# Optimization experiments

Measured on AMD Instinct MI355X. Metric: run time of the kernel, lower is better.

Reference implementation:

```python
import math
import jax, jax.numpy as jnp
import numpy as np

N = 20000      # nodes
E = 320000     # edges
D_IN = 256
D_OUT = 256
H = 8
DK = D_OUT // H  # 32


def setup_inputs() -> dict:
    key = jax.random.key(0)
    ks = jax.random.split(key, 16)
    h = jax.random.normal(ks[0], (N, D_IN), dtype=jnp.float32)
    src = jax.random.randint(ks[1], (E,), 0, N, dtype=jnp.int32)
    dst = jax.random.randint(ks[2], (E,), 0, N, dtype=jnp.int32)
    s = 1.0 / math.sqrt(D_IN)
    Wk = jax.random.uniform(ks[3], (D_OUT, D_IN), jnp.float32, -s, s)
    bk = jnp.zeros((D_OUT,), jnp.float32)
    Wq = jax.random.uniform(ks[4], (D_OUT, D_IN), jnp.float32, -s, s)
    bq = jnp.zeros((D_OUT,), jnp.float32)
    Wv = jax.random.uniform(ks[5], (D_OUT, D_IN), jnp.float32, -s, s)
    bv = jnp.zeros((D_OUT,), jnp.float32)
    so = 1.0 / math.sqrt(D_OUT)
    Wa = jax.random.uniform(ks[6], (D_OUT, D_OUT), jnp.float32, -so, so)
    ba = jnp.zeros((D_OUT,), jnp.float32)
    # xavier_uniform over [n_rel=1, H, DK, DK]; fan_in = fan_out = DK
    bound = math.sqrt(6.0 / (DK + DK))
    rel_att = jax.random.uniform(ks[7], (H, DK, DK), jnp.float32, -bound, bound)
    rel_msg = jax.random.uniform(ks[8], (H, DK, DK), jnp.float32, -bound, bound)
    rel_pri = jnp.ones((H,), jnp.float32)
    skip = jnp.ones((), jnp.float32)
    return {"h": h, "src": src, "dst": dst, "Wk": Wk, "bk": bk, "Wq": Wq,
            "bq": bq, "Wv": Wv, "bv": bv, "Wa": Wa, "ba": ba,
            "rel_att": rel_att, "rel_msg": rel_msg, "rel_pri": rel_pri,
            "skip": skip}


def reference(h, src, dst, Wk, bk, Wq, bq, Wv, bv, Wa, ba, rel_att, rel_msg, rel_pri, skip):
    n = h.shape[0]
    sqrt_dk = math.sqrt(DK)
    # per-node projections, [N, H, DK]
    k = (h @ Wk.T + bk).reshape(n, H, DK)
    q = (h @ Wq.T + bq).reshape(n, H, DK)
    v = (h @ Wv.T + bv).reshape(n, H, DK)
    # relation-specific transforms (single relation, index 0)
    k = jnp.einsum('nhd,hde->nhe', k, rel_att)
    v = jnp.einsum('nhd,hde->nhe', v, rel_msg)
    # edge-wise dot-product score: v_dot_u(q_dst, k_src) -> [E, H]
    score = jnp.einsum('ehd,ehd->eh', q[dst], k[src]) * rel_pri / sqrt_dk
    # edge softmax normalized by dst
    m = jax.ops.segment_max(score, dst, num_segments=n)          # [N, H]
    ex = jnp.exp(score - m[dst])
    z = jax.ops.segment_sum(ex, dst, num_segments=n)             # [N, H]
    attn = ex / z[dst]                                           # [E, H]
    # weighted message aggregation: sum_e attn * v_src -> [N, H, DK]
    agg = jax.ops.segment_sum(v[src] * attn[:, :, None], dst, num_segments=n)
    t = agg.reshape(n, D_OUT)
    trans = t @ Wa.T + ba                                        # dropout = eval identity
    alpha = jax.nn.sigmoid(skip)
    return trans * alpha + h * (1.0 - alpha)
```

## Files before the change

### kernel.cpp

```cpp
#include <hip/hip_runtime.h>
#include <hip/hip_bf16.h>
#include <math.h>


#define NN   20000
#define NE   320000
#define MPAD 20096

typedef unsigned short u16;
typedef unsigned char  u8;
typedef __bf16 bf16x8 __attribute__((ext_vector_type(8)));
typedef u16    u16x8  __attribute__((ext_vector_type(8)));
typedef float  f32x4  __attribute__((ext_vector_type(4)));

__device__ __forceinline__ float bf2f(u16 x) {
    union { float f; unsigned u; } c; c.u = ((unsigned)x) << 16; return c.f;
}
__device__ __forceinline__ u16 f2bf(float f) {
    union { float f; unsigned u; } c; c.f = f;
    unsigned r = c.u + 0x7fffu + ((c.u >> 16) & 1u);
    return (u16)(r >> 16);
}

#if __has_builtin(__builtin_amdgcn_cvt_pk_fp8_f32) && __has_builtin(__builtin_amdgcn_cvt_pk_f32_fp8)
#define HWFP8 1
#else
#define HWFP8 0
#endif

__device__ __forceinline__ u8 f2fp8(float x) {
#if HWFP8
    return (u8)(__builtin_amdgcn_cvt_pk_fp8_f32(x, x, 0, false) & 0xff);
#else
    if (x != x) return 0x7f;
    unsigned sg = (x < 0.f) ? 0x80u : 0u;
    float a = fabsf(x); if (a > 448.f) a = 448.f;
    if (a < 0.015625f) {
        int m = (int)rintf(a * 512.f);
        if (m > 7) return (u8)(sg | 0x08);
        return (u8)(sg | m);
    }
    int e; (void)frexpf(a, &e);
    int p = e - 1;
    float mant = a * exp2f((float)(-p));
    int m = (int)rintf((mant - 1.f) * 8.f);
    int ef = p + 7;
    if (m == 8) { m = 0; ef++; }
    if (ef > 15) { ef = 15; m = 6; }
    return (u8)(sg | (ef << 3) | m);
#endif
}

__device__ __forceinline__ void fp8x4_dec(unsigned w, float* o) {
#if HWFP8
    auto lo = __builtin_amdgcn_cvt_pk_f32_fp8(w, false);
    auto hi = __builtin_amdgcn_cvt_pk_f32_fp8(w, true);
    o[0] = lo[0]; o[1] = lo[1]; o[2] = hi[0]; o[3] = hi[1];
#else
    #pragma unroll
    for (int j = 0; j < 4; ++j) {
        u8 b = (w >> (8 * j)) & 0xff;
        unsigned e = (b >> 3) & 15, m = b & 7;
        float v;
        if (e) { union { unsigned u; float f; } c; c.u = ((e + 120) << 23) | (m << 20); v = c.f; }
        else v = (float)m * 0.001953125f;
        o[j] = (b & 0x80) ? -v : v;
    }
#endif
}

__device__ __forceinline__ float fast_exp2(float x) {
#if __has_builtin(__builtin_amdgcn_exp2f)
    return __builtin_amdgcn_exp2f(x);
#else
    return exp2f(x);
#endif
}

__device__ __forceinline__ void gload_lds16(const void* g, void* l) {
    __builtin_amdgcn_global_load_lds(
        (const __attribute__((address_space(1))) unsigned*)g,
        (__attribute__((address_space(3))) unsigned*)l, 16, 0, 0);
}

__global__ void prep0(const float* __restrict__ Wq, const float* __restrict__ bq,
                      const float* __restrict__ Wk, const float* __restrict__ bk,
                      const float* __restrict__ Wv, const float* __restrict__ bv,
                      const float* __restrict__ Wa,
                      const float* __restrict__ rel_att, const float* __restrict__ rel_msg,
                      const float* __restrict__ rel_pri,
                      u16* __restrict__ W_all, float* __restrict__ b_eff,
                      u16* __restrict__ Wa_bf, int* __restrict__ deg)
{
    const int bid = blockIdx.x, t = threadIdx.x;
    if (bid < 20) {
        const int i = bid * 256 + t;
        if (i < 5024) *(int4*)(deg + i * 4) = make_int4(0, 0, 0, 0);
    } else if (bid < 788) {
        const int row = bid - 20, col = t;
        float val;
        if (row < 256) {
            val = Wq[row * 256 + col];
            if (col == 0) b_eff[row] = bq[row];
        } else {
            const int i = row - 256, g = i >> 7, o = i & 127;
            const bool isk = (o < 64);
            const int d = 64 * g + (isk ? o : o - 64);
            const int hh = d >> 5, e = d & 31;
            if (isk) {
                const float s = rel_pri[hh] * 0.17677669529663687f * 1.4426950408889634f;
                float acc = 0.f;
                for (int dd = 0; dd < 32; ++dd)
                    acc += rel_att[hh * 1024 + dd * 32 + e] * Wk[(hh * 32 + dd) * 256 + col];
                val = acc * s;
                if (col == 0) {
                    float b = 0.f;
                    for (int dd = 0; dd < 32; ++dd) b += rel_att[hh * 1024 + dd * 32 + e] * bk[hh * 32 + dd];
                    b_eff[row] = b * s;
                }
            } else {
                float acc = 0.f;
                for (int dd = 0; dd < 32; ++dd)
                    acc += rel_msg[hh * 1024 + dd * 32 + e] * Wv[(hh * 32 + dd) * 256 + col];
                val = acc;
                if (col == 0) {
                    float b = 0.f;
                    for (int dd = 0; dd < 32; ++dd) b += rel_msg[hh * 1024 + dd * 32 + e] * bv[hh * 32 + dd];
                    b_eff[row] = b;
                }
            }
        }
        W_all[row * 256 + col] = f2bf(val);
    } else {
        const int idx = (bid - 788) * 256 + t;
        Wa_bf[idx] = f2bf(Wa[idx]);
    }
}

__global__ __launch_bounds__(256) void gemm_qkv(
    const float* __restrict__ h, const u16* __restrict__ B,
    const float* __restrict__ bias, const int* __restrict__ dst,
    u16* __restrict__ qb, u8* __restrict__ kv8, int* __restrict__ deg)
{
    if (blockIdx.x >= 960) {
        const int e = (blockIdx.x - 960) * 256 + threadIdx.x;
        if (e < NE) atomicAdd(&deg[dst[e]], 1);
        return;
    }
    const int xcd = blockIdx.x & 7, slot = blockIdx.x >> 3;
    const int rb = (slot % 20) * 8 + xcd;
    const int cb = slot / 20;
    if (rb >= 157) return;
    __shared__ u16 LDS[128 * 128];
    u16* At = LDS;
    u16* Bt = LDS + 128 * 64;
    const int t = threadIdx.x;
    const int wave = t >> 6, lane = t & 63;
    const int row0 = rb * 128, col0 = cb * 128;
    const int wm = (wave >> 1) * 64, wn = (wave & 1) * 64;
    const int cl = lane & 15, rh = lane >> 4;
    const int srow = t >> 3;
    const int lchunk = t & 7;
    const int swz = (t >> 3) & 7;
    const int scol = lchunk * 8;
    const int sc_swz = (lchunk ^ swz) * 8;

    f32x4 acc[4][4] = {};

    for (int k0 = 0; k0 < 256; k0 += 64) {
        __syncthreads();
        #pragma unroll
        for (int r = 0; r < 4; ++r) {
            const int rT = r * 32 + srow;
            const int grow = row0 + rT;
            u16x8 w8 = (u16x8)0;
            if (grow < NN) {
                const float4 f0 = *(const float4*)(h + (size_t)grow * 256 + k0 + scol);
                const float4 f1 = *(const float4*)(h + (size_t)grow * 256 + k0 + scol + 4);
                w8[0] = f2bf(f0.x); w8[1] = f2bf(f0.y); w8[2] = f2bf(f0.z); w8[3] = f2bf(f0.w);
                w8[4] = f2bf(f1.x); w8[5] = f2bf(f1.y); w8[6] = f2bf(f1.z); w8[7] = f2bf(f1.w);
            }
            *(u16x8*)&At[rT * 64 + (lchunk ^ swz) * 8] = w8;
            gload_lds16(B + (size_t)(col0 + rT) * 256 + k0 + sc_swz,
                        &Bt[(r * 256 + wave * 64) * 8]);
        }
        __syncthreads();
        #pragma unroll
        for (int kk = 0; kk < 64; kk += 32) {
            const int kc = kk >> 3;
            bf16x8 af[4], bb[4];
            #pragma unroll
            for (int m = 0; m < 4; ++m) {
                const int ar = wm + 16 * m + cl;
                af[m] = *(const bf16x8*)&At[ar * 64 + (((kc + rh) ^ (ar & 7)) * 8)];
            }
            #pragma unroll
            for (int n = 0; n < 4; ++n) {
                const int br = wn + 16 * n + cl;
                bb[n] = *(const bf16x8*)&Bt[br * 64 + (((kc + rh) ^ (br & 7)) * 8)];
            }
            #pragma unroll
            for (int m = 0; m < 4; ++m)
                #pragma unroll
                for (int n = 0; n < 4; ++n)
                    acc[m][n] = __builtin_amdgcn_mfma_f32_16x16x32_bf16(af[m], bb[n], acc[m][n], 0, 0, 0);
        }
    }

    __syncthreads();
    if (cb < 2) {
        #pragma unroll
        for (int n = 0; n < 4; ++n) {
            const int col = wn + 16 * n + cl;
            const float bv = bias[col0 + col];
            #pragma unroll
            for (int m = 0; m < 4; ++m) {
                const int rowb = wm + 16 * m + 4 * rh;
                #pragma unroll
                for (int r = 0; r < 4; ++r) {
                    const int row = rowb + r;
                    LDS[row * 128 + ((((col >> 3) ^ (row & 15)) << 3) | (col & 7))] =
                        f2bf(acc[m][n][r] + bv);
                }
            }
        }
        __syncthreads();
        #pragma unroll
        for (int it = 0; it < 8; ++it) {
            const int u = it * 256 + t;
            const int row = u >> 4, lc = u & 15;
            *(u16x8*)(qb + (size_t)(row0 + row) * 256 + col0 + lc * 8) =
                *(const u16x8*)&LDS[row * 128 + ((lc ^ (row & 15)) << 3)];
        }
    } else {
        u8* Cs8 = (u8*)LDS;
        const int g = cb - 2;
        #pragma unroll
        for (int n = 0; n < 4; ++n) {
            const int col = wn + 16 * n + cl;
            const float bv = bias[col0 + col];
            const int o = col & 63;
            const int p = ((o >> 3) << 4) + ((col < 64) ? 0 : 8) + (o & 7);
            #pragma unroll
            for (int m = 0; m < 4; ++m) {
                const int rowb = wm + 16 * m + 4 * rh;
                #pragma unroll
                for (int r = 0; r < 4; ++r) {
                    const int row = rowb + r;
                    Cs8[row * 128 + ((((p >> 3) ^ (row & 15)) << 3) | (p & 7))] =
                        f2fp8(acc[m][n][r] + bv);
                }
            }
        }
        __syncthreads();
        #pragma unroll
        for (int it = 0; it < 4; ++it) {
            const int u = it * 256 + t;
            const int row = u >> 3, un = u & 7;
            const uint2 a = *(const uint2*)&Cs8[row * 128 + (((2 * un) ^ (row & 15)) << 3)];
            const uint2 b = *(const uint2*)&Cs8[row * 128 + (((2 * un + 1) ^ (row & 15)) << 3)];
            *(uint4*)(kv8 + (size_t)(row0 + row) * 512 + g * 128 + un * 16) =
                make_uint4(a.x, a.y, b.x, b.y);
        }
    }
}

__global__ __launch_bounds__(256) void gemm_out(
    const u16* __restrict__ A, const u16* __restrict__ B,
    const float* __restrict__ bias, const float* __restrict__ hres,
    const float* __restrict__ skip, float* __restrict__ C)
{
    const int xcd = blockIdx.x & 7, slot = blockIdx.x >> 3;
    const int rb = (slot % 40) * 8 + xcd;
    const int cbo = slot / 40;
    if (rb >= 314) return;
    __shared__ u16 At[64 * 64];
    __shared__ u16 Bt[64 * 64];
    const int t = threadIdx.x;
    const int wave = t >> 6, lane = t & 63;
    const int row0 = rb * 64, col0 = cbo * 64;
    const int wm = (wave >> 1) * 32, wn = (wave & 1) * 32;
    const int cl = lane & 15, rh = lane >> 4;
    const int srow = t >> 3;
    const int sc_swz = (((t & 7) ^ ((t >> 3) & 7))) * 8;

    f32x4 acc[2][2] = {};

    for (int k0 = 0; k0 < 256; k0 += 64) {
        __syncthreads();
        #pragma unroll
        for (int r = 0; r < 2; ++r) {
            const int rowT = r * 32 + srow;
            gload_lds16(A + (size_t)(row0 + rowT) * 256 + k0 + sc_swz, &At[(r * 2048 + wave * 512)]);
            gload_lds16(B + (size_t)(col0 + rowT) * 256 + k0 + sc_swz, &Bt[(r * 2048 + wave * 512)]);
        }
        __syncthreads();
        #pragma unroll
        for (int kk = 0; kk < 64; kk += 32) {
            const int kc = kk >> 3;
            bf16x8 af[2], bb[2];
            #pragma unroll
            for (int m = 0; m < 2; ++m) {
                const int ar = wm + 16 * m + cl;
                af[m] = *(const bf16x8*)&At[ar * 64 + (((kc + rh) ^ (ar & 7)) * 8)];
            }
            #pragma unroll
            for (int n = 0; n < 2; ++n) {
                const int br = wn + 16 * n + cl;
                bb[n] = *(const bf16x8*)&Bt[br * 64 + (((kc + rh) ^ (br & 7)) * 8)];
            }
            #pragma unroll
            for (int m = 0; m < 2; ++m)
                #pragma unroll
                for (int n = 0; n < 2; ++n)
                    acc[m][n] = __builtin_amdgcn_mfma_f32_16x16x32_bf16(af[m], bb[n], acc[m][n], 0, 0, 0);
        }
    }
    const float alpha = 1.f / (1.f + __expf(-skip[0]));
    const float beta = 1.f - alpha;
    #pragma unroll
    for (int n = 0; n < 2; ++n) {
        const int col = col0 + wn + 16 * n + cl;
        const float bv = bias[col];
        #pragma unroll
        for (int m = 0; m < 2; ++m) {
            const int rowb = row0 + wm + 16 * m + 4 * rh;
            #pragma unroll
            for (int r = 0; r < 4; ++r) {
                const int row = rowb + r;
                if (row < NN)
                    C[(size_t)row * 256 + col] =
                        (acc[m][n][r] + bv) * alpha + hres[(size_t)row * 256 + col] * beta;
            }
        }
    }
}

__global__ __launch_bounds__(1024) void scan1(const int* __restrict__ deg,
                                              int* __restrict__ off, int* __restrict__ bsum)
{
    __shared__ int wsum[16];
    __shared__ int wpre[16];
    const int t = threadIdx.x, b = blockIdx.x;
    const int i = b * 1024 + t;
    const int lane = t & 63, wv = t >> 6;
    const int v = (i < NN) ? deg[i] : 0;
    int s = v;
    #pragma unroll
    for (int o = 1; o < 64; o <<= 1) {
        const int u = __shfl_up(s, o);
        if (lane >= o) s += u;
    }
    if (lane == 63) wsum[wv] = s;
    __syncthreads();
    if (wv == 0) {
        const int x = (lane < 16) ? wsum[lane] : 0;
        int sx = x;
        #pragma unroll
        for (int o = 1; o < 16; o <<= 1) {
            const int u = __shfl_up(sx, o);
            if (lane >= o) sx += u;
        }
        if (lane < 16) wpre[lane] = sx - x;
    }
    __syncthreads();
    const int incl = s + wpre[wv];
    if (i < NN) off[i] = incl - v;
    if (t == 1023) bsum[b] = incl;
}

__global__ __launch_bounds__(1024) void scan2(const int* __restrict__ bsum,
                                              int* __restrict__ off, int* __restrict__ cur)
{
    __shared__ int pre;
    const int t = threadIdx.x, b = blockIdx.x;
    const int i = b * 1024 + t;
    if (t == 0) {
        int p = 0;
        for (int j = 0; j < b; ++j) p += bsum[j];
        pre = p;
    }
    __syncthreads();
    if (i < NN) {
        const int o = off[i] + pre;
        off[i] = o; cur[i] = o;
    }
    if (b == 19 && t == 0) off[NN] = pre + bsum[19];
}

__global__ void scatter_edges(const int* __restrict__ dst, const int* __restrict__ src,
                              int* __restrict__ cur, int* __restrict__ esrc)
{
    const int e = blockIdx.x * 256 + threadIdx.x;
    if (e < NE) {
        const int p = atomicAdd(&cur[dst[e]], 1);
        esrc[p] = src[e];
    }
}

__device__ __forceinline__ void agg_edge(const u8* __restrict__ kv8, int id,
                                         const float* qf, int sl, float& z, float* acc)
{
    const uint4 w = *(const uint4*)(kv8 + (size_t)id * 512 + sl * 16);
    float kf[8], vf[8];
    fp8x4_dec(w.x, kf); fp8x4_dec(w.y, kf + 4);
    float s = 0.f;
    #pragma unroll
    for (int j = 0; j < 8; ++j) s += qf[j] * kf[j];
    s += __shfl_xor(s, 1);
    s += __shfl_xor(s, 2);
    const float ex = fast_exp2(s);
    z += ex;
    fp8x4_dec(w.z, vf); fp8x4_dec(w.w, vf + 4);
    #pragma unroll
    for (int j = 0; j < 8; ++j) acc[j] += ex * vf[j];
}

__global__ __launch_bounds__(256) void aggregate(
    const u16* __restrict__ qb, const u8* __restrict__ kv8, const int* __restrict__ off,
    const int* __restrict__ esrc, u16* __restrict__ tout)
{
    const int wid = blockIdx.x * 4 + (threadIdx.x >> 6);
    const int lane = threadIdx.x & 63;
    const int half = lane >> 5, sl = lane & 31;
    if (wid >= MPAD) return;
    if (wid >= NN) {
        if (half == 0) *(u16x8*)(tout + (size_t)wid * 256 + sl * 8) = (u16x8)0;
        return;
    }
    const u16x8 qv = *(const u16x8*)(qb + (size_t)wid * 256 + sl * 8);
    float qf[8];
    #pragma unroll
    for (int j = 0; j < 8; ++j) qf[j] = bf2f(qv[j]);
    float acc[8] = {0.f, 0.f, 0.f, 0.f, 0.f, 0.f, 0.f, 0.f};
    float z = 0.f;
    const int e0 = off[wid], e1 = off[wid + 1];
    for (int c0 = e0; c0 < e1; c0 += 64) {
        const int cnt = min(64, e1 - c0);
        const int jj = c0 + lane;
        const int myid = (jj < e1) ? esrc[jj] : 0;
        for (int i = 0; i < cnt; i += 16) {
            int ii[8], idv[8];
            #pragma unroll
            for (int j = 0; j < 8; ++j) {
                ii[j] = i + 2 * j + half;
                idv[j] = __shfl(myid, ii[j]);
            }
            #pragma unroll
            for (int j = 0; j < 8; ++j)
                if (ii[j] < cnt)
                    agg_edge(kv8, idv[j], qf, sl, z, acc);
        }
    }
    #pragma unroll
    for (int j = 0; j < 8; ++j) acc[j] += __shfl_xor(acc[j], 32);
    z += __shfl_xor(z, 32);
    if (half == 0) {
        const float rz = (z > 0.f) ? 1.f / z : 0.f;
        u16x8 o;
        #pragma unroll
        for (int j = 0; j < 8; ++j) o[j] = f2bf(acc[j] * rz);
        *(u16x8*)(tout + (size_t)wid * 256 + sl * 8) = o;
    }
}

extern "C" void kernel_launch(void* const* d_in, const int* in_sizes, int n_in,
                              void* d_out, int out_size, void* d_ws, size_t ws_size,
                              hipStream_t stream)
{
    const float* h   = (const float*)d_in[0];
    const int*   src = (const int*)d_in[1];
    const int*   dst = (const int*)d_in[2];
    const float* Wk  = (const float*)d_in[3];
    const float* bk  = (const float*)d_in[4];
    const float* Wq  = (const float*)d_in[5];
    const float* bq  = (const float*)d_in[6];
    const float* Wv  = (const float*)d_in[7];
    const float* bv  = (const float*)d_in[8];
    const float* Wa  = (const float*)d_in[9];
    const float* ba  = (const float*)d_in[10];
    const float* rel_att = (const float*)d_in[11];
    const float* rel_msg = (const float*)d_in[12];
    const float* rel_pri = (const float*)d_in[13];
    const float* skip    = (const float*)d_in[14];
    float* out = (float*)d_out;

    char* w = (char*)d_ws;
    u16*   W_all = (u16*)(w + 0);
    float* b_eff = (float*)(w + 393216);
    u16*   Wa_bf = (u16*)(w + 396288);
    u16*   qb    = (u16*)(w + 527360);
    u8*    kv8   = (u8*)(w + 10816512);
    u16*   t_bf  = (u16*)(w + 21105664);
    int*   deg   = (int*)(w + 31394816);
    int*   off   = (int*)(w + 31475200);
    int*   cur   = (int*)(w + 31555584);
    int*   bsum  = (int*)(w + 31635968);
    int*   esrc  = (int*)(w + 31636096);

    prep0<<<1044, 256, 0, stream>>>(Wq, bq, Wk, bk, Wv, bv, Wa,
                                    rel_att, rel_msg, rel_pri,
                                    W_all, b_eff, Wa_bf, deg);
    gemm_qkv<<<960 + 1250, 256, 0, stream>>>(h, W_all, b_eff, dst, qb, kv8, deg);
    scan1<<<20, 1024, 0, stream>>>(deg, off, bsum);
    scan2<<<20, 1024, 0, stream>>>(bsum, off, cur);
    scatter_edges<<<NE / 256, 256, 0, stream>>>(dst, src, cur, esrc);
    aggregate<<<MPAD / 4, 256, 0, stream>>>(qb, kv8, off, esrc, t_bf);
    gemm_out<<<1280, 256, 0, stream>>>(t_bf, Wa_bf, ba, h, skip, out);
}
```

Before: 107.6 us.

## Double-buffer LDS tiles in QKV and output GEMMs, move degree count to prep

Both GEMM kernels now prefetch the next K-slice into a second LDS buffer while MFMAs run on the current one, which removes one barrier per iteration and overlaps global loads with compute. The degree histogram atomics move from the QKV GEMM launch into the prep kernel, and the degree buffer is cleared with a memset instead of prep blocks. The QKV GEMM doubles its LDS footprint to 64KB, which may reduce occupancy, and the memset adds an extra queued operation.

```diff
diff --git a/kernel.cpp b/kernel.cpp
--- a/kernel.cpp
+++ b/kernel.cpp
@@ -88,16 +88,13 @@
                       const float* __restrict__ Wv, const float* __restrict__ bv,
                       const float* __restrict__ Wa,
                       const float* __restrict__ rel_att, const float* __restrict__ rel_msg,
-                      const float* __restrict__ rel_pri,
+                      const float* __restrict__ rel_pri, const int* __restrict__ dst,
                       u16* __restrict__ W_all, float* __restrict__ b_eff,
                       u16* __restrict__ Wa_bf, int* __restrict__ deg)
 {
     const int bid = blockIdx.x, t = threadIdx.x;
-    if (bid < 20) {
-        const int i = bid * 256 + t;
-        if (i < 5024) *(int4*)(deg + i * 4) = make_int4(0, 0, 0, 0);
-    } else if (bid < 788) {
-        const int row = bid - 20, col = t;
+    if (bid < 768) {
+        const int row = bid, col = t;
         float val;
         if (row < 256) {
             val = Wq[row * 256 + col];
@@ -131,29 +128,24 @@
             }
         }
         W_all[row * 256 + col] = f2bf(val);
+    } else if (bid < 1024) {
+        const int idx = (bid - 768) * 256 + t;
+        Wa_bf[idx] = f2bf(Wa[idx]);
     } else {
-        const int idx = (bid - 788) * 256 + t;
-        Wa_bf[idx] = f2bf(Wa[idx]);
+        const int e = (bid - 1024) * 256 + t;
+        if (e < NE) atomicAdd(&deg[dst[e]], 1);
     }
 }
 
 __global__ __launch_bounds__(256) void gemm_qkv(
     const float* __restrict__ h, const u16* __restrict__ B,
-    const float* __restrict__ bias, const int* __restrict__ dst,
-    u16* __restrict__ qb, u8* __restrict__ kv8, int* __restrict__ deg)
-{
-    if (blockIdx.x >= 960) {
-        const int e = (blockIdx.x - 960) * 256 + threadIdx.x;
-        if (e < NE) atomicAdd(&deg[dst[e]], 1);
-        return;
-    }
+    const float* __restrict__ bias, u16* __restrict__ qb, u8* __restrict__ kv8)
+{
     const int xcd = blockIdx.x & 7, slot = blockIdx.x >> 3;
     const int rb = (slot % 20) * 8 + xcd;
     const int cb = slot / 20;
     if (rb >= 157) return;
-    __shared__ u16 LDS[128 * 128];
-    u16* At = LDS;
-    u16* Bt = LDS + 128 * 64;
+    __shared__ u16 LDS[32768];
     const int t = threadIdx.x;
     const int wave = t >> 6, lane = t & 63;
     const int row0 = rb * 128, col0 = cb * 128;
@@ -166,28 +158,55 @@
     const int sc_swz = (lchunk ^ swz) * 8;
 
     f32x4 acc[4][4] = {};
-
-    for (int k0 = 0; k0 < 256; k0 += 64) {
-        __syncthreads();
-        #pragma unroll
-        for (int r = 0; r < 4; ++r) {
-            const int rT = r * 32 + srow;
-            const int grow = row0 + rT;
-            u16x8 w8 = (u16x8)0;
-            if (grow < NN) {
-                const float4 f0 = *(const float4*)(h + (size_t)grow * 256 + k0 + scol);
-                const float4 f1 = *(const float4*)(h + (size_t)grow * 256 + k0 + scol + 4);
-                w8[0] = f2bf(f0.x); w8[1] = f2bf(f0.y); w8[2] = f2bf(f0.z); w8[3] = f2bf(f0.w);
-                w8[4] = f2bf(f1.x); w8[5] = f2bf(f1.y); w8[6] = f2bf(f1.z); w8[7] = f2bf(f1.w);
-            }
-            *(u16x8*)&At[rT * 64 + (lchunk ^ swz) * 8] = w8;
-            gload_lds16(B + (size_t)(col0 + rT) * 256 + k0 + sc_swz,
-                        &Bt[(r * 256 + wave * 64) * 8]);
-        }
-        __syncthreads();
-        #pragma unroll
-        for (int kk = 0; kk < 64; kk += 32) {
-            const int kc = kk >> 3;
+    float4 fa[4][2];
+
+    #pragma unroll
+    for (int r = 0; r < 4; ++r) {
+        const int grow = row0 + r * 32 + srow;
+        if (grow < NN) {
+            fa[r][0] = *(const float4*)(h + (size_t)grow * 256 + scol);
+            fa[r][1] = *(const float4*)(h + (size_t)grow * 256 + scol + 4);
+        } else {
+            fa[r][0] = make_float4(0.f, 0.f, 0.f, 0.f);
+            fa[r][1] = make_float4(0.f, 0.f, 0.f, 0.f);
+        }
+        gload_lds16(B + (size_t)(col0 + r * 32 + srow) * 256 + sc_swz,
+                    &LDS[8192 + (r * 256 + wave * 64) * 8]);
+    }
+    #pragma unroll
+    for (int r = 0; r < 4; ++r) {
+        u16x8 w8;
+        w8[0] = f2bf(fa[r][0].x); w8[1] = f2bf(fa[r][0].y); w8[2] = f2bf(fa[r][0].z); w8[3] = f2bf(fa[r][0].w);
+        w8[4] = f2bf(fa[r][1].x); w8[5] = f2bf(fa[r][1].y); w8[6] = f2bf(fa[r][1].z); w8[7] = f2bf(fa[r][1].w);
+        *(u16x8*)&LDS[(r * 32 + srow) * 64 + (lchunk ^ swz) * 8] = w8;
+    }
+    __syncthreads();
+
+    #pragma unroll
+    for (int ki = 0; ki < 4; ++ki) {
+        const int boff = (ki & 1) * 16384;
+        const int nboff = boff ^ 16384;
+        if (ki < 3) {
+            const int k0n = (ki + 1) * 64;
+            #pragma unroll
+            for (int r = 0; r < 4; ++r) {
+                const int grow = row0 + r * 32 + srow;
+                if (grow < NN) {
+                    fa[r][0] = *(const float4*)(h + (size_t)grow * 256 + k0n + scol);
+                    fa[r][1] = *(const float4*)(h + (size_t)grow * 256 + k0n + scol + 4);
+                } else {
+                    fa[r][0] = make_float4(0.f, 0.f, 0.f, 0.f);
+                    fa[r][1] = make_float4(0.f, 0.f, 0.f, 0.f);
+                }
+                gload_lds16(B + (size_t)(col0 + r * 32 + srow) * 256 + k0n + sc_swz,
+                            &LDS[nboff + 8192 + (r * 256 + wave * 64) * 8]);
+            }
+        }
+        const u16* At = &LDS[boff];
+        const u16* Bt = &LDS[boff + 8192];
+        #pragma unroll
+        for (int kk = 0; kk < 2; ++kk) {
+            const int kc = kk * 4;
             bf16x8 af[4], bb[4];
             #pragma unroll
             for (int m = 0; m < 4; ++m) {
@@ -205,9 +224,18 @@
                 for (int n = 0; n < 4; ++n)
                     acc[m][n] = __builtin_amdgcn_mfma_f32_16x16x32_bf16(af[m], bb[n], acc[m][n], 0, 0, 0);
         }
-    }
-
-    __syncthreads();
+        if (ki < 3) {
+            #pragma unroll
+            for (int r = 0; r < 4; ++r) {
+                u16x8 w8;
+                w8[0] = f2bf(fa[r][0].x); w8[1] = f2bf(fa[r][0].y); w8[2] = f2bf(fa[r][0].z); w8[3] = f2bf(fa[r][0].w);
+                w8[4] = f2bf(fa[r][1].x); w8[5] = f2bf(fa[r][1].y); w8[6] = f2bf(fa[r][1].z); w8[7] = f2bf(fa[r][1].w);
+                *(u16x8*)&LDS[nboff + (r * 32 + srow) * 64 + (lchunk ^ swz) * 8] = w8;
+            }
+        }
+        __syncthreads();
+    }
+
     if (cb < 2) {
         #pragma unroll
         for (int n = 0; n < 4; ++n) {
@@ -272,32 +300,46 @@
 {
     const int xcd = blockIdx.x & 7, slot = blockIdx.x >> 3;
     const int rb = (slot % 40) * 8 + xcd;
-    const int cbo = slot / 40;
+    const int cb = slot / 40;
     if (rb >= 314) return;
-    __shared__ u16 At[64 * 64];
-    __shared__ u16 Bt[64 * 64];
+    __shared__ u16 LDS[16384];
     const int t = threadIdx.x;
     const int wave = t >> 6, lane = t & 63;
-    const int row0 = rb * 64, col0 = cbo * 64;
+    const int row0 = rb * 64, col0 = cb * 64;
     const int wm = (wave >> 1) * 32, wn = (wave & 1) * 32;
     const int cl = lane & 15, rh = lane >> 4;
     const int srow = t >> 3;
     const int sc_swz = (((t & 7) ^ ((t >> 3) & 7))) * 8;
 
+    #pragma unroll
+    for (int r = 0; r < 2; ++r) {
+        const int rowT = r * 32 + srow;
+        gload_lds16(A + (size_t)(row0 + rowT) * 256 + sc_swz, &LDS[(r * 2048 + wave * 512)]);
+        gload_lds16(B + (size_t)(col0 + rowT) * 256 + sc_swz, &LDS[4096 + (r * 2048 + wave * 512)]);
+    }
+    __syncthreads();
+
     f32x4 acc[2][2] = {};
-
-    for (int k0 = 0; k0 < 256; k0 += 64) {
-        __syncthreads();
-        #pragma unroll
-        for (int r = 0; r < 2; ++r) {
-            const int rowT = r * 32 + srow;
-            gload_lds16(A + (size_t)(row0 + rowT) * 256 + k0 + sc_swz, &At[(r * 2048 + wave * 512)]);
-            gload_lds16(B + (size_t)(col0 + rowT) * 256 + k0 + sc_swz, &Bt[(r * 2048 + wave * 512)]);
-        }
-        __syncthreads();
-        #pragma unroll
-        for (int kk = 0; kk < 64; kk += 32) {
-            const int kc = kk >> 3;
+    #pragma unroll
+    for (int ki = 0; ki < 4; ++ki) {
+        const int boff = (ki & 1) * 8192;
+        const int nboff = boff ^ 8192;
+        if (ki < 3) {
+            const int k0n = (ki + 1) * 64;
+            #pragma unroll
+            for (int r = 0; r < 2; ++r) {
+                const int rowT = r * 32 + srow;
+                gload_lds16(A + (size_t)(row0 + rowT) * 256 + k0n + sc_swz,
+                            &LDS[nboff + (r * 2048 + wave * 512)]);
+                gload_lds16(B + (size_t)(col0 + rowT) * 256 + k0n + sc_swz,
+                            &LDS[nboff + 4096 + (r * 2048 + wave * 512)]);
+            }
+        }
+        const u16* At = &LDS[boff];
+        const u16* Bt = &LDS[boff + 4096];
+        #pragma unroll
+        for (int kk = 0; kk < 2; ++kk) {
+            const int kc = kk * 4;
             bf16x8 af[2], bb[2];
             #pragma unroll
             for (int m = 0; m < 2; ++m) {
@@ -315,6 +357,7 @@
                 for (int n = 0; n < 2; ++n)
                     acc[m][n] = __builtin_amdgcn_mfma_f32_16x16x32_bf16(af[m], bb[n], acc[m][n], 0, 0, 0);
         }
+        __syncthreads();
     }
     const float alpha = 1.f / (1.f + __expf(-skip[0]));
     const float beta = 1.f - alpha;
@@ -498,10 +541,11 @@
     int*   bsum  = (int*)(w + 31635968);
     int*   esrc  = (int*)(w + 31636096);
 
-    prep0<<<1044, 256, 0, stream>>>(Wq, bq, Wk, bk, Wv, bv, Wa,
-                                    rel_att, rel_msg, rel_pri,
-                                    W_all, b_eff, Wa_bf, deg);
-    gemm_qkv<<<960 + 1250, 256, 0, stream>>>(h, W_all, b_eff, dst, qb, kv8, deg);
+    (void)hipMemsetAsync(deg, 0, NN * sizeof(int), stream);
+    prep0<<<1024 + 1250, 256, 0, stream>>>(Wq, bq, Wk, bk, Wv, bv, Wa,
+                                           rel_att, rel_msg, rel_pri, dst,
+                                           W_all, b_eff, Wa_bf, deg);
+    gemm_qkv<<<960, 256, 0, stream>>>(h, W_all, b_eff, qb, kv8);
     scan1<<<20, 1024, 0, stream>>>(deg, off, bsum);
     scan2<<<20, 1024, 0, stream>>>(bsum, off, cur);
     scatter_edges<<<NE / 256, 256, 0, stream>>>(dst, src, cur, esrc);
```

Result: slower. 115.1 us (+7.0%).

## Register-prefetch next K tile in both GEMMs to overlap loads with MFMA

Applied to the files above, without the earlier changes.

Both the fused projection GEMM and the output GEMM drop the direct global-to-LDS loads. Each K step now prefetches the next 64-wide tile into registers, runs the MFMAs on the current LDS tile, then writes the prefetched data into LDS with the same XOR swizzle. The aim is to hide global load latency behind compute instead of stalling at a barrier on every K step. In exchange it raises register pressure, since fp32 A values and bf16 B vectors stay live across the MFMA loop, and it adds a barrier around each LDS commit.

```diff
diff --git a/kernel.cpp b/kernel.cpp
--- a/kernel.cpp
+++ b/kernel.cpp
@@ -75,12 +75,6 @@
 #else
     return exp2f(x);
 #endif
-}
-
-__device__ __forceinline__ void gload_lds16(const void* g, void* l) {
-    __builtin_amdgcn_global_load_lds(
-        (const __attribute__((address_space(1))) unsigned*)g,
-        (__attribute__((address_space(3))) unsigned*)l, 16, 0, 0);
 }
 
 __global__ void prep0(const float* __restrict__ Wq, const float* __restrict__ bq,
@@ -161,33 +155,46 @@
     const int cl = lane & 15, rh = lane >> 4;
     const int srow = t >> 3;
     const int lchunk = t & 7;
-    const int swz = (t >> 3) & 7;
-    const int scol = lchunk * 8;
-    const int sc_swz = (lchunk ^ swz) * 8;
+    const int swz = srow & 7;
 
     f32x4 acc[4][4] = {};
-
-    for (int k0 = 0; k0 < 256; k0 += 64) {
-        __syncthreads();
+    float4 a0[4], a1[4];
+    u16x8 bz[4];
+
+    auto LOAD = [&](int k0) {
         #pragma unroll
         for (int r = 0; r < 4; ++r) {
-            const int rT = r * 32 + srow;
-            const int grow = row0 + rT;
-            u16x8 w8 = (u16x8)0;
+            const int grow = row0 + r * 32 + srow;
             if (grow < NN) {
-                const float4 f0 = *(const float4*)(h + (size_t)grow * 256 + k0 + scol);
-                const float4 f1 = *(const float4*)(h + (size_t)grow * 256 + k0 + scol + 4);
-                w8[0] = f2bf(f0.x); w8[1] = f2bf(f0.y); w8[2] = f2bf(f0.z); w8[3] = f2bf(f0.w);
-                w8[4] = f2bf(f1.x); w8[5] = f2bf(f1.y); w8[6] = f2bf(f1.z); w8[7] = f2bf(f1.w);
-            }
-            *(u16x8*)&At[rT * 64 + (lchunk ^ swz) * 8] = w8;
-            gload_lds16(B + (size_t)(col0 + rT) * 256 + k0 + sc_swz,
-                        &Bt[(r * 256 + wave * 64) * 8]);
-        }
-        __syncthreads();
-        #pragma unroll
-        for (int kk = 0; kk < 64; kk += 32) {
-            const int kc = kk >> 3;
+                a0[r] = *(const float4*)(h + (size_t)grow * 256 + k0 + lchunk * 8);
+                a1[r] = *(const float4*)(h + (size_t)grow * 256 + k0 + lchunk * 8 + 4);
+            } else {
+                a0[r] = make_float4(0.f, 0.f, 0.f, 0.f);
+                a1[r] = make_float4(0.f, 0.f, 0.f, 0.f);
+            }
+            bz[r] = *(const u16x8*)(B + (size_t)(col0 + r * 32 + srow) * 256 + k0 + lchunk * 8);
+        }
+    };
+    auto COMMIT = [&]() {
+        #pragma unroll
+        for (int r = 0; r < 4; ++r) {
+            u16x8 w8;
+            w8[0] = f2bf(a0[r].x); w8[1] = f2bf(a0[r].y); w8[2] = f2bf(a0[r].z); w8[3] = f2bf(a0[r].w);
+            w8[4] = f2bf(a1[r].x); w8[5] = f2bf(a1[r].y); w8[6] = f2bf(a1[r].z); w8[7] = f2bf(a1[r].w);
+            *(u16x8*)&At[(r * 32 + srow) * 64 + (lchunk ^ swz) * 8] = w8;
+            *(u16x8*)&Bt[(r * 32 + srow) * 64 + (lchunk ^ swz) * 8] = bz[r];
+        }
+    };
+
+    LOAD(0);
+    COMMIT();
+    __syncthreads();
+    #pragma unroll
+    for (int ki = 0; ki < 4; ++ki) {
+        if (ki < 3) LOAD((ki + 1) * 64);
+        #pragma unroll
+        for (int kk = 0; kk < 2; ++kk) {
+            const int kc = kk * 4;
             bf16x8 af[4], bb[4];
             #pragma unroll
             for (int m = 0; m < 4; ++m) {
@@ -205,9 +212,13 @@
                 for (int n = 0; n < 4; ++n)
                     acc[m][n] = __builtin_amdgcn_mfma_f32_16x16x32_bf16(af[m], bb[n], acc[m][n], 0, 0, 0);
         }
-    }
-
-    __syncthreads();
+        __syncthreads();
+        if (ki < 3) {
+            COMMIT();
+            __syncthreads();
+        }
+    }
+
     if (cb < 2) {
         #pragma unroll
         for (int n = 0; n < 4; ++n) {
@@ -282,22 +293,36 @@
     const int wm = (wave >> 1) * 32, wn = (wave & 1) * 32;
     const int cl = lane & 15, rh = lane >> 4;
     const int srow = t >> 3;
-    const int sc_swz = (((t & 7) ^ ((t >> 3) & 7))) * 8;
+    const int lchunk = t & 7;
+    const int swz = srow & 7;
 
     f32x4 acc[2][2] = {};
-
-    for (int k0 = 0; k0 < 256; k0 += 64) {
-        __syncthreads();
+    u16x8 az[2], bz[2];
+
+    auto LOAD = [&](int k0) {
         #pragma unroll
         for (int r = 0; r < 2; ++r) {
-            const int rowT = r * 32 + srow;
-            gload_lds16(A + (size_t)(row0 + rowT) * 256 + k0 + sc_swz, &At[(r * 2048 + wave * 512)]);
-            gload_lds16(B + (size_t)(col0 + rowT) * 256 + k0 + sc_swz, &Bt[(r * 2048 + wave * 512)]);
-        }
-        __syncthreads();
-        #pragma unroll
-        for (int kk = 0; kk < 64; kk += 32) {
-            const int kc = kk >> 3;
+            az[r] = *(const u16x8*)(A + (size_t)(row0 + r * 32 + srow) * 256 + k0 + lchunk * 8);
+            bz[r] = *(const u16x8*)(B + (size_t)(col0 + r * 32 + srow) * 256 + k0 + lchunk * 8);
+        }
+    };
+    auto COMMIT = [&]() {
+        #pragma unroll
+        for (int r = 0; r < 2; ++r) {
+            *(u16x8*)&At[(r * 32 + srow) * 64 + (lchunk ^ swz) * 8] = az[r];
+            *(u16x8*)&Bt[(r * 32 + srow) * 64 + (lchunk ^ swz) * 8] = bz[r];
+        }
+    };
+
+    LOAD(0);
+    COMMIT();
+    __syncthreads();
+    #pragma unroll
+    for (int ki = 0; ki < 4; ++ki) {
+        if (ki < 3) LOAD((ki + 1) * 64);
+        #pragma unroll
+        for (int kk = 0; kk < 2; ++kk) {
+            const int kc = kk * 4;
             bf16x8 af[2], bb[2];
             #pragma unroll
             for (int m = 0; m < 2; ++m) {
@@ -314,6 +339,11 @@
                 #pragma unroll
                 for (int n = 0; n < 2; ++n)
                     acc[m][n] = __builtin_amdgcn_mfma_f32_16x16x32_bf16(af[m], bb[n], acc[m][n], 0, 0, 0);
+        }
+        __syncthreads();
+        if (ki < 3) {
+            COMMIT();
+            __syncthreads();
         }
     }
     const float alpha = 1.f / (1.f + __expf(-skip[0]));
```

New measurement: 104.0 us. -3.3%, faster.
